# Performance work log

Measured on AMD Instinct MI355X. Metric: run time of the kernel, lower is better.

Reference implementation:

```python
import jax, jax.numpy as jnp
from jax import lax
import numpy as np

K_IN, K_OUT, H, ML = 32, 16, 256, 80
L_PRE, L_FWD, B = 60, 80, 1024


def gru_cell(x, h, Wih, Whh, bih, bhh):
    # torch GRU gate order: r, z, n
    gi = x @ Wih.T + bih
    gh = h @ Whh.T + bhh
    ir, iz, inn = jnp.split(gi, 3, axis=-1)
    hr, hz, hn = jnp.split(gh, 3, axis=-1)
    r = jax.nn.sigmoid(ir + hr)
    z = jax.nn.sigmoid(iz + hz)
    n = jnp.tanh(inn + r * hn)
    return (1.0 - z) * n + z * h


def setup_inputs() -> dict:
    key = jax.random.key(0)
    ks = jax.random.split(key, 24)
    s = 0.05
    rn = lambda k, shp: (jax.random.normal(k, shp) * s).astype(jnp.float32)
    inp = {
        "pre_x": jax.random.normal(ks[0], (L_PRE, B, K_IN), dtype=jnp.float32),
        "pre_y": jax.random.normal(ks[1], (L_PRE, B, K_OUT), dtype=jnp.float32),
        "forward_x": jax.random.normal(ks[2], (L_FWD, B, K_IN), dtype=jnp.float32),
        # encoder: embedding Linear(k_in+k_out -> H), GRU(H,H)
        "enc_emb_W": rn(ks[3], (H, K_IN + K_OUT)),
        "enc_emb_b": rn(ks[4], (H,)),
        "enc_Wih": rn(ks[5], (3 * H, H)),
        "enc_Whh": rn(ks[6], (3 * H, H)),
        "enc_bih": rn(ks[7], (3 * H,)),
        "enc_bhh": rn(ks[8], (3 * H,)),
        # decoder: embedding Linear(k_out+k_in -> H), attn Linear(2H -> ML),
        # attn_combine Linear(2H -> H), GRU(H,H), out Linear(H -> k_out)
        "dec_emb_W": rn(ks[9], (H, K_OUT + K_IN)),
        "dec_emb_b": rn(ks[10], (H,)),
        "attn_W": rn(ks[11], (ML, 2 * H)),
        "attn_b": rn(ks[12], (ML,)),
        "comb_W": rn(ks[13], (H, 2 * H)),
        "comb_b": rn(ks[14], (H,)),
        "dec_Wih": rn(ks[15], (3 * H, H)),
        "dec_Whh": rn(ks[16], (3 * H, H)),
        "dec_bih": rn(ks[17], (3 * H,)),
        "dec_bhh": rn(ks[18], (3 * H,)),
        "out_W": rn(ks[19], (K_OUT, H)),
        "out_b": rn(ks[20], (K_OUT,)),
    }
    return inp


def reference(pre_x, pre_y, forward_x,
              enc_emb_W, enc_emb_b, enc_Wih, enc_Whh, enc_bih, enc_bhh,
              dec_emb_W, dec_emb_b, attn_W, attn_b, comb_W, comb_b,
              dec_Wih, dec_Whh, dec_bih, dec_bhh, out_W, out_b):
    L_pre, batch, _ = pre_x.shape
    hdim = enc_emb_b.shape[0]
    max_len = attn_b.shape[0]

    # ---- encoder ----
    emb = jnp.concatenate([pre_x, pre_y], axis=2) @ enc_emb_W.T + enc_emb_b  # [L_pre,B,H]
    h0 = jnp.zeros((batch, hdim), dtype=pre_x.dtype)

    def enc_step(h, x):
        h2 = gru_cell(x, h, enc_Wih, enc_Whh, enc_bih, enc_bhh)
        return h2, h2

    enc_h, enc_outs = lax.scan(enc_step, h0, emb)
    # pad encoder outputs to max_length along time (zeros beyond L_pre)
    enc_outputs = jnp.zeros((max_len, batch, hdim), dtype=pre_x.dtype).at[:L_pre].set(enc_outs)
    enc_bmh = enc_outputs.transpose(1, 0, 2)  # [B, ML, H]

    # ---- decoder (dropout inactive: eval mode) ----
    def dec_step(carry, fx):
        y, h = carry
        di = jnp.concatenate([y, fx], axis=-1)            # [B, k_out+k_in]
        e = di @ dec_emb_W.T + dec_emb_b                   # [B, H]
        logits = jnp.concatenate([e, h], axis=-1) @ attn_W.T + attn_b  # [B, ML]
        aw = jax.nn.softmax(logits, axis=-1)
        ctx = jnp.einsum('bm,bmh->bh', aw, enc_bmh)        # [B, H]
        g = jnp.tanh(jnp.concatenate([e, ctx], axis=-1) @ comb_W.T + comb_b)
        h2 = gru_cell(g, h, dec_Wih, dec_Whh, dec_bih, dec_bhh)
        y2 = h2 @ out_W.T + out_b                          # [B, k_out]
        return (y2, h2), y2

    y_init = jnp.zeros_like(pre_y[0])
    _, ys = lax.scan(dec_step, (y_init, enc_h), forward_x)
    return ys  # [L_fwd, B, k_out]
```

## Files before the change

### kernel.cpp

```cpp
#include <hip/hip_runtime.h>
#include <hip/hip_bf16.h>

#define BATCH 1024
#define HD 256
#define MLEN 80
#define LPRE 60
#define LFWD 80
#define KIN 32
#define KOUT 16

typedef unsigned short bf16_t;
typedef __attribute__((ext_vector_type(8))) short bf16x8;
typedef __attribute__((ext_vector_type(4))) float f32x4;
typedef __attribute__((ext_vector_type(4))) unsigned u32x4;

#define MFMA __builtin_amdgcn_mfma_f32_16x16x32_bf16

__device__ __forceinline__ float bf2f(bf16_t v){ return __uint_as_float(((unsigned)v)<<16); }
__device__ __forceinline__ bf16_t f2bf(float f){
    unsigned u = __float_as_uint(f);
    return (bf16_t)((u + 0x7FFFu + ((u>>16)&1u)) >> 16);
}
__device__ __forceinline__ unsigned pack2(float lo, float hi){
    return (unsigned)f2bf(lo) | ((unsigned)f2bf(hi)<<16);
}
__device__ __forceinline__ float bflo(unsigned d){ return __uint_as_float(d<<16); }
__device__ __forceinline__ float bfhi(unsigned d){ return __uint_as_float(d & 0xffff0000u); }
__device__ __forceinline__ float sigm(float x){ return 1.0f/(1.0f+__expf(-x)); }

#define OFF_Z  262144
#define OFF_IN 524288
#define OFF_HN 655360

__global__ void pack_gru(const float* __restrict__ Wih, const float* __restrict__ Whh,
                         bf16_t* __restrict__ dst)
{
    int T = blockIdx.x*256 + threadIdx.x;
    int grp, local;
    if (T < 16384){ grp=0; local=T; }
    else if (T < 32768){ grp=1; local=T-16384; }
    else if (T < 40960){ grp=2; local=T-32768; }
    else { grp=3; local=T-40960; }
    int nkt = (grp<2)?16:8;
    int nt  = local / (nkt*64);
    int rem = local - nt*(nkt*64);
    int kt  = rem >> 6;
    int l   = rem & 63;
    int n   = nt*16 + (l&15);
    int k0  = kt*32 + ((l>>4)<<3);
    unsigned w[4];
    #pragma unroll
    for (int h2=0; h2<4; h2++){
        float v[2];
        #pragma unroll
        for (int s=0; s<2; s++){
            int k = k0 + h2*2 + s;
            if (grp==0)      v[s] = (k<256)? Wih[(size_t)n*HD + k]       : Whh[(size_t)n*HD + (k-256)];
            else if (grp==1) v[s] = (k<256)? Wih[(size_t)(256+n)*HD + k] : Whh[(size_t)(256+n)*HD + (k-256)];
            else if (grp==2) v[s] = Wih[(size_t)(512+n)*HD + k];
            else             v[s] = Whh[(size_t)(512+n)*HD + k];
        }
        w[h2] = pack2(v[0], v[1]);
    }
    uint4 u = {w[0],w[1],w[2],w[3]};
    *(uint4*)((char*)dst + (size_t)T*16) = u;
}

__global__ void pack_B512(const float* __restrict__ W, bf16_t* __restrict__ dst)
{
    int T = blockIdx.x*256 + threadIdx.x;
    int nt = T >> 10, kt = (T>>6)&15, l = T&63;
    int n = nt*16 + (l&15);
    int k0 = kt*32 + ((l>>4)<<3);
    unsigned w[4];
    #pragma unroll
    for (int h2=0; h2<4; h2++)
        w[h2] = pack2(W[(size_t)n*512 + k0+h2*2], W[(size_t)n*512 + k0+h2*2+1]);
    uint4 u = {w[0],w[1],w[2],w[3]};
    *(uint4*)((char*)dst + (size_t)T*16) = u;
}

__global__ void wfuse_kernel(const float* __restrict__ dembW, const float* __restrict__ dembB,
                             const float* __restrict__ outW, const float* __restrict__ outB,
                             float* __restrict__ Wfuse, float* __restrict__ ebias)
{
    int T = blockIdx.x*256 + threadIdx.x;
    if (T < 65536){
        int k = T >> 8, n = T & 255;
        float acc = 0.f;
        #pragma unroll
        for (int o=0;o<16;o++) acc += dembW[(size_t)n*48 + o]*outW[(size_t)o*HD + k];
        Wfuse[(size_t)k*HD + n] = acc;
    } else if (T < 65792){
        int n = T - 65536;
        float acc = dembB[n];
        #pragma unroll
        for (int o=0;o<16;o++) acc += outB[o]*dembW[(size_t)n*48 + o];
        ebias[n] = acc;
    }
}

__global__ void pack_logits(const float* __restrict__ Wfuse, const float* __restrict__ dembW,
                            const float* __restrict__ attW, const float* __restrict__ attB,
                            const float* __restrict__ dembB, const float* __restrict__ ebias,
                            bf16_t* __restrict__ BL, bf16_t* __restrict__ BL0,
                            float* __restrict__ lb, float* __restrict__ lb0)
{
    int T = blockIdx.x*256 + threadIdx.x;
    if (T < 5760){
        int variant = (T < 2880) ? 0 : 1;
        int local = variant ? (T-2880) : T;
        int nt = local/576, rem = local - nt*576;
        int kt = rem >> 6, l = rem & 63;
        int m  = nt*16 + (l&15);
        int k0 = kt*32 + ((l>>4)<<3);
        float acc[8];
        if (kt < 8){
            #pragma unroll
            for (int d=0;d<8;d++) acc[d] = attW[(size_t)m*512 + 256 + k0 + d];
            if (variant == 0){
                const float* ar = attW + (size_t)m*512;
                for (int n=0;n<256;n+=4){
                    float4 w = *(const float4*)(ar + n);
                    #pragma unroll
                    for (int d=0;d<8;d++){
                        float4 f = *(const float4*)(Wfuse + (size_t)(k0+d)*HD + n);
                        acc[d] = fmaf(f.x, w.x, acc[d]);
                        acc[d] = fmaf(f.y, w.y, acc[d]);
                        acc[d] = fmaf(f.z, w.z, acc[d]);
                        acc[d] = fmaf(f.w, w.w, acc[d]);
                    }
                }
            }
        } else {
            int kp0 = k0 - 256;
            #pragma unroll
            for (int d=0;d<8;d++) acc[d] = 0.f;
            const float* ar = attW + (size_t)m*512;
            for (int n=0;n<256;n++){
                float w = ar[n];
                const float* dr = dembW + (size_t)n*48 + 16 + kp0;
                float4 d0 = *(const float4*)dr;
                float4 d1 = *(const float4*)(dr+4);
                acc[0]=fmaf(d0.x,w,acc[0]); acc[1]=fmaf(d0.y,w,acc[1]);
                acc[2]=fmaf(d0.z,w,acc[2]); acc[3]=fmaf(d0.w,w,acc[3]);
                acc[4]=fmaf(d1.x,w,acc[4]); acc[5]=fmaf(d1.y,w,acc[5]);
                acc[6]=fmaf(d1.z,w,acc[6]); acc[7]=fmaf(d1.w,w,acc[7]);
            }
        }
        unsigned w4[4];
        #pragma unroll
        for (int h2=0;h2<4;h2++) w4[h2] = pack2(acc[h2*2], acc[h2*2+1]);
        uint4 u = {w4[0],w4[1],w4[2],w4[3]};
        bf16_t* d = variant ? BL0 : BL;
        *(uint4*)((char*)d + (size_t)local*16) = u;
    } else if (T < 5840){
        int m = T - 5760;
        float acc = attB[m];
        const float* ar = attW + (size_t)m*512;
        for (int n=0;n<256;n+=4){
            float4 w = *(const float4*)(ar + n);
            float4 e = *(const float4*)(ebias + n);
            acc = fmaf(e.x,w.x,acc); acc = fmaf(e.y,w.y,acc);
            acc = fmaf(e.z,w.z,acc); acc = fmaf(e.w,w.w,acc);
        }
        lb[m] = acc;
    } else if (T < 5920){
        int m = T - 5840;
        float acc = attB[m];
        const float* ar = attW + (size_t)m*512;
        for (int n=0;n<256;n+=4){
            float4 w = *(const float4*)(ar + n);
            float4 e = *(const float4*)(dembB + n);
            acc = fmaf(e.x,w.x,acc); acc = fmaf(e.y,w.y,acc);
            acc = fmaf(e.z,w.z,acc); acc = fmaf(e.w,w.w,acc);
        }
        lb0[m] = acc;
    }
}

__global__ void pack_gfold(const float* __restrict__ Wfuse, const float* __restrict__ dembW,
                           const float* __restrict__ combW, const float* __restrict__ combB,
                           const float* __restrict__ ebias, const float* __restrict__ dembB,
                           bf16_t* __restrict__ dst, float* __restrict__ cbf, float* __restrict__ cbf0)
{
    int T = blockIdx.x*256 + threadIdx.x;
    if (T < 9216){
        int nt = T/576, rem = T - nt*576;
        int kt = rem >> 6, l = rem & 63;
        int n = nt*16 + (l&15);
        int k0 = kt*32 + ((l>>4)<<3);
        float acc[8];
        #pragma unroll
        for (int d=0;d<8;d++) acc[d] = 0.f;
        const float* wr = combW + (size_t)n*512;
        if (kt < 8){
            for (int j=0;j<256;j+=4){
                float4 w = *(const float4*)(wr + j);
                #pragma unroll
                for (int d=0;d<8;d++){
                    float4 f = *(const float4*)(Wfuse + (size_t)(k0+d)*HD + j);
                    acc[d] = fmaf(f.x, w.x, acc[d]);
                    acc[d] = fmaf(f.y, w.y, acc[d]);
                    acc[d] = fmaf(f.z, w.z, acc[d]);
                    acc[d] = fmaf(f.w, w.w, acc[d]);
                }
            }
        } else {
            int kp0 = k0 - 256;
            for (int j=0;j<256;j++){
                float w = wr[j];
                const float* dr = dembW + (size_t)j*48 + 16 + kp0;
                float4 d0 = *(const float4*)dr;
                float4 d1 = *(const float4*)(dr+4);
                acc[0]=fmaf(d0.x,w,acc[0]); acc[1]=fmaf(d0.y,w,acc[1]);
                acc[2]=fmaf(d0.z,w,acc[2]); acc[3]=fmaf(d0.w,w,acc[3]);
                acc[4]=fmaf(d1.x,w,acc[4]); acc[5]=fmaf(d1.y,w,acc[5]);
                acc[6]=fmaf(d1.z,w,acc[6]); acc[7]=fmaf(d1.w,w,acc[7]);
            }
        }
        unsigned w4[4];
        #pragma unroll
        for (int h2=0;h2<4;h2++) w4[h2] = pack2(acc[h2*2], acc[h2*2+1]);
        uint4 u = {w4[0],w4[1],w4[2],w4[3]};
        *(uint4*)((char*)dst + (size_t)T*16) = u;
    } else if (T < 9472){
        int n = T - 9216;
        float acc = combB[n];
        const float* wr = combW + (size_t)n*512;
        for (int j=0;j<256;j+=4){
            float4 w = *(const float4*)(wr + j);
            float4 e = *(const float4*)(ebias + j);
            acc = fmaf(e.x,w.x,acc); acc = fmaf(e.y,w.y,acc);
            acc = fmaf(e.z,w.z,acc); acc = fmaf(e.w,w.w,acc);
        }
        cbf[n] = acc;
    } else if (T < 9728){
        int n = T - 9472;
        float acc = combB[n];
        const float* wr = combW + (size_t)n*512;
        for (int j=0;j<256;j+=4){
            float4 w = *(const float4*)(wr + j);
            float4 e = *(const float4*)(dembB + j);
            acc = fmaf(e.x,w.x,acc); acc = fmaf(e.y,w.y,acc);
            acc = fmaf(e.z,w.z,acc); acc = fmaf(e.w,w.w,acc);
        }
        cbf0[n] = acc;
    }
}

__global__ void pack_out(const float* __restrict__ outW, bf16_t* __restrict__ dst)
{
    int T = blockIdx.x*256 + threadIdx.x;
    int kt = T >> 6, l = T & 63;
    int n  = l & 15;
    int k0 = kt*32 + ((l>>4)<<3);
    unsigned w[4];
    #pragma unroll
    for (int h2=0; h2<4; h2++)
        w[h2] = pack2(outW[(size_t)n*HD + k0+h2*2], outW[(size_t)n*HD + k0+h2*2+1]);
    uint4 u = {w[0],w[1],w[2],w[3]};
    *(uint4*)((char*)dst + (size_t)T*16) = u;
}

__global__ __launch_bounds__(256) void emb_kernel(
    const float* __restrict__ px, const float* __restrict__ py,
    const float* __restrict__ embW, const float* __restrict__ embB,
    bf16_t* __restrict__ emb)
{
    __shared__ float Ws[256*49];
    __shared__ float xy[16][48];
    __shared__ float bs[256];
    int t = blockIdx.y, b0 = blockIdx.x*16, tid = threadIdx.x;
    for (int i = tid; i < 256*48; i += 256){ int n=i/48, k=i-n*48; Ws[n*49+k]=embW[i]; }
    bs[tid] = embB[tid];
    for (int i = tid; i < 16*48; i += 256){
        int r=i/48, k=i-r*48;
        xy[r][k] = (k<KIN)? px[((size_t)t*BATCH + b0+r)*KIN + k]
                          : py[((size_t)t*BATCH + b0+r)*KOUT + (k-KIN)];
    }
    __syncthreads();
    int n = tid;
    const float* w = &Ws[n*49];
    for (int r=0;r<16;r++){
        float acc = bs[n];
        #pragma unroll
        for (int k=0;k<48;k++) acc += xy[r][k]*w[k];
        emb[((size_t)t*BATCH + b0+r)*HD + n] = f2bf(acc);
    }
}

__global__ void fxconv(const float* __restrict__ fx, bf16_t* __restrict__ dst)
{
    size_t i = (size_t)blockIdx.x*256 + threadIdx.x;
    const float4* s = (const float4*)(fx + i*8);
    float4 a = s[0], b = s[1];
    uint4 u = { pack2(a.x,a.y), pack2(a.z,a.w), pack2(b.x,b.y), pack2(b.z,b.w) };
    *(uint4*)(dst + i*8) = u;
}

__global__ __launch_bounds__(256) void pgemm(
    const bf16_t* __restrict__ enc, const bf16_t* __restrict__ Bcmb,
    bf16_t* __restrict__ P)
{
    __shared__ __align__(16) bf16_t As[16][264];
    __shared__ __align__(16) bf16_t Gs[16][264];
    int tid = threadIdx.x, b0 = blockIdx.x*16, t = blockIdx.y;
    const bf16_t* src = enc + ((size_t)t*BATCH + b0)*HD;
    for (int i = tid; i < 512; i += 256){
        int r = i>>5, c = i&31;
        *(uint4*)&As[r][c*8] = *(const uint4*)(src + (size_t)r*HD + c*8);
    }
    __syncthreads();
    int lane = tid&63, wave = tid>>6;
    const bf16_t* arow = &As[lane&15][(lane>>4)*8];
    size_t loff = (size_t)lane*16;
    #pragma unroll
    for (int u=0; u<4; u++){
        int nt = wave*4 + u;
        f32x4 c = {0,0,0,0};
        #pragma unroll
        for (int k8=0; k8<8; k8++){
            bf16x8 a = *(const bf16x8*)(arow + k8*32);
            bf16x8 b = *(const bf16x8*)((const char*)Bcmb + (size_t)(((nt<<4)+8+k8)<<10) + loff);
            c = MFMA(a, b, c, 0,0,0);
        }
        int n = (nt<<4) + (lane&15);
        #pragma unroll
        for (int q=0;q<4;q++) Gs[((lane>>4)<<2)+q][n] = f2bf(c[q]);
    }
    __syncthreads();
    bf16_t* dst = P + ((size_t)t*BATCH + b0)*HD;
    for (int i = tid; i < 512; i += 256){
        int r = i>>5, c = i&31;
        *(uint4*)(dst + (size_t)r*HD + c*8) = *(const uint4*)&Gs[r][c*8];
    }
}

__global__ __launch_bounds__(512) void gru_step2(
    const bf16_t* __restrict__ A0, const bf16_t* __restrict__ A1,
    const bf16_t* __restrict__ Bp,
    const float* __restrict__ bih, const float* __restrict__ bhh,
    const float* __restrict__ hprev, float* __restrict__ hnext,
    bf16_t* __restrict__ hnext_bf, bf16_t* __restrict__ extra_bf)
{
    __shared__ __align__(16) bf16_t As[16][520];
    __shared__ __align__(16) f32x4 redR[4][64];
    __shared__ __align__(16) f32x4 redZ[4][64];
    __shared__ __align__(16) f32x4 redI[4][64];
    int tid = threadIdx.x, b0 = blockIdx.x*16;
    for (int i = tid; i < 1024; i += 512){
        int r = i>>6, c = i&63;
        const bf16_t* src = (c<32)? (A0 + (size_t)(b0+r)*HD + c*8)
                                  : (A1 + (size_t)(b0+r)*HD + (c-32)*8);
        *(uint4*)&As[r][c*8] = *(const uint4*)src;
    }
    __syncthreads();
    int lane = tid & 63, wave = tid >> 6;
    int pairId = wave >> 1, half = wave & 1;
    int jt = blockIdx.y*4 + pairId;
    const char* arow = (const char*)&As[lane&15][(lane>>4)*8];
    const char* bpc = (const char*)Bp;
    size_t loff = (size_t)lane*16;
    size_t offX = half ? (size_t)OFF_HN : (size_t)OFF_IN;
    int kt0 = half*8;
    f32x4 cr={0,0,0,0}, cz={0,0,0,0}, cx={0,0,0,0};
    #pragma unroll
    for (int k8=0; k8<8; k8++){
        int kt = kt0 + k8;
        bf16x8 a  = *(const bf16x8*)(arow + kt*64);
        bf16x8 br = *(const bf16x8*)(bpc + (size_t)(((jt<<4)+kt)<<10) + loff);
        bf16x8 bz = *(const bf16x8*)(bpc + OFF_Z + (size_t)(((jt<<4)+kt)<<10) + loff);
        bf16x8 bx = *(const bf16x8*)(bpc + offX + (size_t)(((jt<<3)+k8)<<10) + loff);
        cr = MFMA(a, br, cr, 0,0,0);
        cz = MFMA(a, bz, cz, 0,0,0);
        cx = MFMA(a, bx, cx, 0,0,0);
    }
    if (half == 0){
        redR[pairId][lane] = cr;
        redZ[pairId][lane] = cz;
        redI[pairId][lane] = cx;
    }
    __syncthreads();
    if (half == 1){
        f32x4 crA = redR[pairId][lane];
        f32x4 czA = redZ[pairId][lane];
        f32x4 ci  = redI[pairId][lane];
        int j = (jt<<4) + (lane&15);
        float b_r = bih[j] + bhh[j];
        float b_z = bih[256+j] + bhh[256+j];
        float b_i = bih[512+j], b_h = bhh[512+j];
        #pragma unroll
        for (int q=0;q<4;q++){
            int b = b0 + ((lane>>4)<<2) + q;
            float rv = sigm(cr[q] + crA[q] + b_r);
            float zv = sigm(cz[q] + czA[q] + b_z);
            float nv = tanhf(ci[q] + b_i + rv*(cx[q] + b_h));
            float h2 = (1.0f - zv)*nv + zv*hprev[(size_t)b*HD + j];
            hnext[(size_t)b*HD + j] = h2;
            bf16_t hb = f2bf(h2);
            hnext_bf[(size_t)b*HD + j] = hb;
            extra_bf[(size_t)b*HD + j] = hb;
        }
    }
}

__global__ __launch_bounds__(1024) void dec_front(
    const bf16_t* __restrict__ hbf, const bf16_t* __restrict__ fxt,
    const bf16_t* __restrict__ P,
    const bf16_t* __restrict__ BL, const bf16_t* __restrict__ Bgf,
    const bf16_t* __restrict__ Bout,
    const float* __restrict__ lbp, const float* __restrict__ cbf,
    const float* __restrict__ outB,
    int t, bf16_t* __restrict__ g_out, float* __restrict__ out)
{
    __shared__ __align__(16) bf16_t As[16][296];
    __shared__ float awL[16][84];
    __shared__ float Cpart[16][256];
    __shared__ float CbF[16][260];

    int tid = threadIdx.x, b0 = blockIdx.x*16;

    if (tid < 576){
        int r = tid/36, c = tid - r*36;
        const bf16_t* src = (c<32)? (hbf + (size_t)(b0+r)*HD + c*8)
                                  : (fxt + (size_t)(b0+r)*KIN + (c-32)*8);
        *(uint4*)&As[r][c*8] = *(const uint4*)src;
    }

    int half = tid >> 9;
    int u    = tid & 511;
    int cr_  = u >> 5;
    int cc0  = (u & 31) * 8;
    const bf16_t* cbp = P + ((size_t)(half*30)*BATCH + (b0+cr_))*HD + cc0;
    u32x4 pf[10];
    #pragma unroll
    for (int i=0;i<10;i++) pf[i] = *(const u32x4*)(cbp + (size_t)i*BATCH*HD);

    __syncthreads();

    int lane = tid & 63, wave = tid >> 6;
    const bf16_t* arow = &As[lane&15][(lane>>4)*8];
    size_t loff = (size_t)lane*16;
    int kt0 = t ? 0 : 8;

    if (wave < 5){
        f32x4 c = {0,0,0,0};
        #pragma unroll
        for (int kt = 0; kt < 9; kt++){
            bf16x8 a = *(const bf16x8*)(arow + kt*32);
            bf16x8 b = *(const bf16x8*)((const char*)BL + (size_t)((wave*9+kt)<<10) + loff);
            c = MFMA(a, b, c, 0,0,0);
        }
        int m = (wave<<4) + (lane&15);
        float bbm = lbp[m];
        #pragma unroll
        for (int q=0;q<4;q++) awL[((lane>>4)<<2)+q][m] = c[q] + bbm;
    } else if (wave == 5 && t > 0){
        f32x4 c = {0,0,0,0};
        #pragma unroll
        for (int kt = 0; kt < 8; kt++){
            bf16x8 a = *(const bf16x8*)(arow + kt*32);
            bf16x8 b = *(const bf16x8*)((const char*)Bout + (size_t)(kt<<10) + loff);
            c = MFMA(a, b, c, 0,0,0);
        }
        int o = lane & 15;
        float bo = outB[o];
        #pragma unroll
        for (int q=0;q<4;q++){
            int r = ((lane>>4)<<2) + q;
            out[((size_t)(t-1)*BATCH + b0+r)*KOUT + o] = c[q] + bo;
        }
    }
    __syncthreads();

    if (tid < 256){
        int r2 = tid >> 4, l2 = tid & 15;
        float vmax = -1e30f;
        for (int m=l2; m<80; m+=16) vmax = fmaxf(vmax, awL[r2][m]);
        #pragma unroll
        for (int k=1; k<16; k<<=1) vmax = fmaxf(vmax, __shfl_xor(vmax, k, 16));
        float ps = 0.f;
        for (int m=l2; m<80; m+=16){ float v = __expf(awL[r2][m]-vmax); awL[r2][m]=v; ps += v; }
        #pragma unroll
        for (int k=1; k<16; k<<=1) ps += __shfl_xor(ps, k, 16);
        float inv = 1.0f/ps;
        for (int m=l2; m<80; m+=16) awL[r2][m] *= inv;
    }
    __syncthreads();

    float acc[8];
    #pragma unroll
    for (int i=0;i<8;i++) acc[i] = 0.f;
    {
        const float* awr = &awL[cr_][half*30];
        #pragma unroll
        for (int i=0;i<10;i++){
            float w = awr[i];
            acc[0]=fmaf(w,bflo(pf[i][0]),acc[0]); acc[1]=fmaf(w,bfhi(pf[i][0]),acc[1]);
            acc[2]=fmaf(w,bflo(pf[i][1]),acc[2]); acc[3]=fmaf(w,bfhi(pf[i][1]),acc[3]);
            acc[4]=fmaf(w,bflo(pf[i][2]),acc[4]); acc[5]=fmaf(w,bfhi(pf[i][2]),acc[5]);
            acc[6]=fmaf(w,bflo(pf[i][3]),acc[6]); acc[7]=fmaf(w,bfhi(pf[i][3]),acc[7]);
        }
        #pragma unroll 5
        for (int i=10;i<30;i++){
            u32x4 v = *(const u32x4*)(cbp + (size_t)i*BATCH*HD);
            float w = awr[i];
            acc[0]=fmaf(w,bflo(v[0]),acc[0]); acc[1]=fmaf(w,bfhi(v[0]),acc[1]);
            acc[2]=fmaf(w,bflo(v[1]),acc[2]); acc[3]=fmaf(w,bfhi(v[1]),acc[3]);
            acc[4]=fmaf(w,bflo(v[2]),acc[4]); acc[5]=fmaf(w,bfhi(v[2]),acc[5]);
            acc[6]=fmaf(w,bflo(v[3]),acc[6]); acc[7]=fmaf(w,bfhi(v[3]),acc[7]);
        }
    }
    if (half == 0){
        float4 p0 = {acc[0],acc[1],acc[2],acc[3]};
        float4 p1 = {acc[4],acc[5],acc[6],acc[7]};
        *(float4*)&Cpart[cr_][cc0]   = p0;
        *(float4*)&Cpart[cr_][cc0+4] = p1;
    }
    __syncthreads();

    if (half == 1){
        float4 p0 = *(const float4*)&Cpart[cr_][cc0];
        float4 p1 = *(const float4*)&Cpart[cr_][cc0+4];
        float4 o0 = {acc[0]+p0.x, acc[1]+p0.y, acc[2]+p0.z, acc[3]+p0.w};
        float4 o1 = {acc[4]+p1.x, acc[5]+p1.y, acc[6]+p1.z, acc[7]+p1.w};
        *(float4*)&CbF[cr_][cc0]   = o0;
        *(float4*)&CbF[cr_][cc0+4] = o1;
    }
    __syncthreads();

    {
        f32x4 c = {0,0,0,0};
        for (int kt=kt0; kt<9; kt++){
            bf16x8 a = *(const bf16x8*)(arow + kt*32);
            bf16x8 b = *(const bf16x8*)((const char*)Bgf + (size_t)((wave*9+kt)<<10) + loff);
            c = MFMA(a, b, c, 0,0,0);
        }
        int n = (wave<<4) + (lane&15);
        float bb = cbf[n];
        #pragma unroll
        for (int q=0;q<4;q++){
            int r = ((lane>>4)<<2) + q;
            g_out[(size_t)(b0+r)*HD + n] = f2bf(tanhf(c[q] + CbF[r][n] + bb));
        }
    }
}

__global__ __launch_bounds__(256) void final79(
    const float* __restrict__ hf, const float* __restrict__ outW,
    const float* __restrict__ outB, float* __restrict__ ys)
{
    __shared__ float hs[16][260];
    __shared__ float ow[16*260];
    int tid = threadIdx.x, b0 = blockIdx.x*16;
    for (int i=tid;i<4096;i+=256){ int o2=i>>8,k=i&255; ow[o2*260+k]=outW[(size_t)o2*HD+k]; }
    for (int i=tid;i<4096;i+=256){ int r=i>>8,k=i&255; hs[r][k]=hf[(size_t)(b0+r)*HD+k]; }
    __syncthreads();
    int r=tid>>4, o=tid&15;
    float acc=outB[o];
    const float* w=&ow[o*260];
    for(int k=0;k<256;k++) acc += hs[r][k]*w[k];
    ys[((size_t)79*BATCH + b0+r)*KOUT + o] = acc;
}

extern "C" void kernel_launch(void* const* d_in, const int* in_sizes, int n_in,
                              void* d_out, int out_size, void* d_ws, size_t ws_size,
                              hipStream_t stream) {
    const float* pre_x    = (const float*)d_in[0];
    const float* pre_y    = (const float*)d_in[1];
    const float* fwd_x    = (const float*)d_in[2];
    const float* enc_embW = (const float*)d_in[3];
    const float* enc_embB = (const float*)d_in[4];
    const float* enc_Wih  = (const float*)d_in[5];
    const float* enc_Whh  = (const float*)d_in[6];
    const float* enc_bih  = (const float*)d_in[7];
    const float* enc_bhh  = (const float*)d_in[8];
    const float* dec_embW = (const float*)d_in[9];
    const float* dec_embB = (const float*)d_in[10];
    const float* attn_W   = (const float*)d_in[11];
    const float* attn_b   = (const float*)d_in[12];
    const float* comb_W   = (const float*)d_in[13];
    const float* comb_b   = (const float*)d_in[14];
    const float* dec_Wih  = (const float*)d_in[15];
    const float* dec_Whh  = (const float*)d_in[16];
    const float* dec_bih  = (const float*)d_in[17];
    const float* dec_bhh  = (const float*)d_in[18];
    const float* out_W    = (const float*)d_in[19];
    const float* out_b    = (const float*)d_in[20];
    float* out = (float*)d_out;

    char* ws = (char*)d_ws;
    size_t o = 0;
    auto alloc = [&](size_t bytes)->char*{
        char* p = ws + o; o = (o + bytes + 255) & ~(size_t)255; return p;
    };
    bf16_t* EMB     = (bf16_t*)alloc((size_t)LPRE*BATCH*HD*2);
    bf16_t* ENC_OUT = (bf16_t*)alloc((size_t)LPRE*BATCH*HD*2);
    bf16_t* PBUF    = (bf16_t*)alloc((size_t)LPRE*BATCH*HD*2);
    bf16_t* FXB     = (bf16_t*)alloc((size_t)LFWD*BATCH*KIN*2);
    float*  HF0     = (float*) alloc((size_t)BATCH*HD*4);
    float*  HF1     = (float*) alloc((size_t)BATCH*HD*4);
    bf16_t* HB0     = (bf16_t*)alloc((size_t)BATCH*HD*2);
    bf16_t* HB1     = (bf16_t*)alloc((size_t)BATCH*HD*2);
    bf16_t* GBUF    = (bf16_t*)alloc((size_t)BATCH*HD*2);
    bf16_t* DUMMY   = (bf16_t*)alloc((size_t)BATCH*HD*2);
    float*  WFUSE   = (float*) alloc((size_t)256*256*4);
    float*  EBIAS   = (float*) alloc(256*4);
    float*  LB      = (float*) alloc(80*4);
    float*  LB0     = (float*) alloc(80*4);
    float*  CBF     = (float*) alloc(256*4);
    float*  CBF0    = (float*) alloc(256*4);
    bf16_t* PACK_ENC = (bf16_t*)alloc(786432);
    bf16_t* PACK_DEC = (bf16_t*)alloc(786432);
    bf16_t* PACK_CMB = (bf16_t*)alloc(262144);
    bf16_t* PACK_GF  = (bf16_t*)alloc(147456);
    bf16_t* PACK_BL  = (bf16_t*)alloc(46080);
    bf16_t* PACK_BL0 = (bf16_t*)alloc(46080);
    bf16_t* PACK_OUT = (bf16_t*)alloc(8192);

    hipMemsetAsync(HF0, 0, (size_t)BATCH*HD*4, stream);
    hipMemsetAsync(HB0, 0, (size_t)BATCH*HD*2, stream);

    dim3 blk(256);
    emb_kernel<<<dim3(64,60), blk, 0, stream>>>(pre_x, pre_y, enc_embW, enc_embB, EMB);
    fxconv<<<dim3(1280), blk, 0, stream>>>(fwd_x, FXB);
    pack_gru<<<dim3(192), blk, 0, stream>>>(enc_Wih, enc_Whh, PACK_ENC);
    pack_gru<<<dim3(192), blk, 0, stream>>>(dec_Wih, dec_Whh, PACK_DEC);
    pack_B512<<<dim3(64), blk, 0, stream>>>(comb_W, PACK_CMB);
    wfuse_kernel<<<dim3(257), blk, 0, stream>>>(dec_embW, dec_embB, out_W, out_b, WFUSE, EBIAS);
    pack_logits<<<dim3(24), blk, 0, stream>>>(WFUSE, dec_embW, attn_W, attn_b, dec_embB,
                                              EBIAS, PACK_BL, PACK_BL0, LB, LB0);
    pack_gfold<<<dim3(38), blk, 0, stream>>>(WFUSE, dec_embW, comb_W, comb_b,
                                             EBIAS, dec_embB, PACK_GF, CBF, CBF0);
    pack_out<<<dim3(2), blk, 0, stream>>>(out_W, PACK_OUT);

    float*  HF[2] = {HF0, HF1};
    bf16_t* HB[2] = {HB0, HB1};
    int p = 0;

    for (int t = 0; t < LPRE; t++){
        gru_step2<<<dim3(64,4), dim3(512), 0, stream>>>(
            EMB + (size_t)t*BATCH*HD, HB[p], PACK_ENC, enc_bih, enc_bhh,
            HF[p], HF[p^1], HB[p^1], ENC_OUT + (size_t)t*BATCH*HD);
        p ^= 1;
    }
    pgemm<<<dim3(64,60), blk, 0, stream>>>(ENC_OUT, PACK_CMB, PBUF);

    for (int t = 0; t < LFWD; t++){
        const bf16_t* fxt = FXB + (size_t)t*BATCH*KIN;
        dec_front<<<dim3(64), dim3(1024), 0, stream>>>(
            HB[p], fxt, PBUF,
            t ? PACK_BL : PACK_BL0, PACK_GF, PACK_OUT,
            t ? LB : LB0, t ? CBF : CBF0, out_b,
            t, GBUF, out);
        gru_step2<<<dim3(64,4), dim3(512), 0, stream>>>(
            GBUF, HB[p], PACK_DEC, dec_bih, dec_bhh,
            HF[p], HF[p^1], HB[p^1], DUMMY);
        p ^= 1;
    }
    final79<<<dim3(64), blk, 0, stream>>>(HF[p], out_W, out_b, out);
}
```

Baseline: 2.275 ms.

## Fuse encoder GRU time loop into one persistent kernel with state in LDS

Replaces the per-timestep encoder GRU launches with a single persistent kernel in which each block owns 16 batch rows for all 60 steps. The hidden state stays in shared memory (fp32 and bf16 copies), and the next step's embedding row is loaded into LDS. This removes 60 kernel launches and the global round-trips of the hidden state. The cost is less parallelism: only 64 blocks, each re-streaming the full packed GRU weights from L2 every step.

```diff
diff --git a/kernel.cpp b/kernel.cpp
--- a/kernel.cpp
+++ b/kernel.cpp
@@ -299,6 +299,87 @@
     *(uint4*)(dst + i*8) = u;
 }
 
+__global__ __launch_bounds__(1024) void enc_persist(
+    const bf16_t* __restrict__ EMB, const bf16_t* __restrict__ Bp,
+    const float* __restrict__ bih, const float* __restrict__ bhh,
+    float* __restrict__ hf_out, bf16_t* __restrict__ hb_out,
+    bf16_t* __restrict__ enc_out)
+{
+    __shared__ __align__(16) bf16_t Xb[16][264];
+    __shared__ __align__(16) bf16_t Hb[16][264];
+    __shared__ float Hf[16][260];
+    int tid = threadIdx.x, b0 = blockIdx.x*16;
+    int lane = tid & 63, wave = tid >> 6;
+    size_t loff = (size_t)lane*16;
+    const char* bpc = (const char*)Bp;
+
+    for (int i = tid; i < 16*264; i += 1024) ((bf16_t*)Hb)[i] = 0;
+    for (int i = tid; i < 16*260; i += 1024) ((float*)Hf)[i] = 0.f;
+    if (tid < 512){
+        int r = tid >> 5, c0 = (tid & 31)*8;
+        *(uint4*)&Xb[r][c0] = *(const uint4*)&EMB[((size_t)0*BATCH + b0+r)*HD + c0];
+    }
+    __syncthreads();
+
+    int jt = wave;
+    int j = (jt<<4) + (lane&15);
+    float b_r = bih[j] + bhh[j];
+    float b_z = bih[256+j] + bhh[256+j];
+    float b_i = bih[512+j], b_h = bhh[512+j];
+    const bf16_t* ar = &Xb[lane&15][(lane>>4)*8];
+    const bf16_t* ah = &Hb[lane&15][(lane>>4)*8];
+
+    #pragma unroll 1
+    for (int t = 0; t < LPRE; t++){
+        f32x4 cr={0,0,0,0}, cz={0,0,0,0}, ci={0,0,0,0}, ch={0,0,0,0};
+        #pragma unroll
+        for (int kt=0; kt<16; kt++){
+            bf16x8 a = (kt<8)? *(const bf16x8*)(ar + kt*32)
+                             : *(const bf16x8*)(ah + (kt-8)*32);
+            bf16x8 br = *(const bf16x8*)(bpc + (size_t)(((jt<<4)+kt)<<10) + loff);
+            bf16x8 bz = *(const bf16x8*)(bpc + OFF_Z + (size_t)(((jt<<4)+kt)<<10) + loff);
+            cr = MFMA(a, br, cr, 0,0,0);
+            cz = MFMA(a, bz, cz, 0,0,0);
+            if (kt < 8){
+                bf16x8 bi = *(const bf16x8*)(bpc + OFF_IN + (size_t)(((jt<<3)+kt)<<10) + loff);
+                ci = MFMA(a, bi, ci, 0,0,0);
+            } else {
+                bf16x8 bh2 = *(const bf16x8*)(bpc + OFF_HN + (size_t)(((jt<<3)+kt-8)<<10) + loff);
+                ch = MFMA(a, bh2, ch, 0,0,0);
+            }
+        }
+        __syncthreads();
+        #pragma unroll
+        for (int q=0;q<4;q++){
+            int r = ((lane>>4)<<2) + q;
+            float rv = sigm(cr[q] + b_r);
+            float zv = sigm(cz[q] + b_z);
+            float nv = tanhf(ci[q] + b_i + rv*(ch[q] + b_h));
+            float h2 = (1.0f - zv)*nv + zv*Hf[r][j];
+            Hf[r][j] = h2;
+            Hb[r][j] = f2bf(h2);
+        }
+        __syncthreads();
+        if (tid < 512){
+            int r = tid >> 5, c0 = (tid & 31)*8;
+            *(uint4*)(enc_out + ((size_t)t*BATCH + b0+r)*HD + c0) = *(const uint4*)&Hb[r][c0];
+            if (t+1 < LPRE)
+                *(uint4*)&Xb[r][c0] = *(const uint4*)&EMB[((size_t)(t+1)*BATCH + b0+r)*HD + c0];
+        }
+        __syncthreads();
+    }
+
+    if (tid < 512){
+        int r = tid >> 5, c0 = (tid & 31)*8;
+        *(uint4*)&hb_out[(size_t)(b0+r)*HD + c0] = *(const uint4*)&Hb[r][c0];
+    }
+    {
+        int r = tid >> 6, c0 = (tid & 63)*4;
+        float4 v = {Hf[r][c0], Hf[r][c0+1], Hf[r][c0+2], Hf[r][c0+3]};
+        *(float4*)&hf_out[(size_t)(b0+r)*HD + c0] = v;
+    }
+}
+
 __global__ __launch_bounds__(256) void pgemm(
     const bf16_t* __restrict__ enc, const bf16_t* __restrict__ Bcmb,
     bf16_t* __restrict__ P)
@@ -619,9 +700,6 @@
     bf16_t* PACK_BL0 = (bf16_t*)alloc(46080);
     bf16_t* PACK_OUT = (bf16_t*)alloc(8192);
 
-    hipMemsetAsync(HF0, 0, (size_t)BATCH*HD*4, stream);
-    hipMemsetAsync(HB0, 0, (size_t)BATCH*HD*2, stream);
-
     dim3 blk(256);
     emb_kernel<<<dim3(64,60), blk, 0, stream>>>(pre_x, pre_y, enc_embW, enc_embB, EMB);
     fxconv<<<dim3(1280), blk, 0, stream>>>(fwd_x, FXB);
@@ -635,17 +713,14 @@
                                              EBIAS, dec_embB, PACK_GF, CBF, CBF0);
     pack_out<<<dim3(2), blk, 0, stream>>>(out_W, PACK_OUT);
 
+    enc_persist<<<dim3(64), dim3(1024), 0, stream>>>(
+        EMB, PACK_ENC, enc_bih, enc_bhh, HF0, HB0, ENC_OUT);
+
+    pgemm<<<dim3(64,60), blk, 0, stream>>>(ENC_OUT, PACK_CMB, PBUF);
+
     float*  HF[2] = {HF0, HF1};
     bf16_t* HB[2] = {HB0, HB1};
     int p = 0;
-
-    for (int t = 0; t < LPRE; t++){
-        gru_step2<<<dim3(64,4), dim3(512), 0, stream>>>(
-            EMB + (size_t)t*BATCH*HD, HB[p], PACK_ENC, enc_bih, enc_bhh,
-            HF[p], HF[p^1], HB[p^1], ENC_OUT + (size_t)t*BATCH*HD);
-        p ^= 1;
-    }
-    pgemm<<<dim3(64,60), blk, 0, stream>>>(ENC_OUT, PACK_CMB, PBUF);
 
     for (int t = 0; t < LFWD; t++){
         const bf16_t* fxt = FXB + (size_t)t*BATCH*KIN;
```

New measurement: 2.770 ms. 1.22x slower.

## Split decoder front kernel across two column-half blocks per batch tile

Applied to the files above, without the earlier changes.

The decoder front kernel now launches a 64x2 grid, with each block handling half of the 256 hidden columns for the context accumulation and the combine GEMM. The attention logits and softmax are recomputed redundantly in both blocks, and only the y==0 block writes the output projection. This doubles the number of blocks in flight (64 blocks underfill the GPU) and halves per-thread context loads, at the cost of duplicated attention work and half the waves sitting idle in the final MFMA stage.

```diff
diff --git a/kernel.cpp b/kernel.cpp
--- a/kernel.cpp
+++ b/kernel.cpp
@@ -405,7 +405,7 @@
     }
 }
 
-__global__ __launch_bounds__(1024) void dec_front(
+__global__ __launch_bounds__(1024) void dec_front2(
     const bf16_t* __restrict__ hbf, const bf16_t* __restrict__ fxt,
     const bf16_t* __restrict__ P,
     const bf16_t* __restrict__ BL, const bf16_t* __restrict__ Bgf,
@@ -416,10 +416,10 @@
 {
     __shared__ __align__(16) bf16_t As[16][296];
     __shared__ float awL[16][84];
-    __shared__ float Cpart[16][256];
-    __shared__ float CbF[16][260];
-
-    int tid = threadIdx.x, b0 = blockIdx.x*16;
+    __shared__ float Cpart[16][128];
+    __shared__ float CbF[16][132];
+
+    int tid = threadIdx.x, b0 = blockIdx.x*16, y = blockIdx.y;
 
     if (tid < 576){
         int r = tid/36, c = tid - r*36;
@@ -431,11 +431,11 @@
     int half = tid >> 9;
     int u    = tid & 511;
     int cr_  = u >> 5;
-    int cc0  = (u & 31) * 8;
-    const bf16_t* cbp = P + ((size_t)(half*30)*BATCH + (b0+cr_))*HD + cc0;
-    u32x4 pf[10];
+    int cl4  = (u & 31) * 4;
+    const bf16_t* cbp = P + ((size_t)(half*30)*BATCH + (b0+cr_))*HD + y*128 + cl4;
+    uint2 pf[10];
     #pragma unroll
-    for (int i=0;i<10;i++) pf[i] = *(const u32x4*)(cbp + (size_t)i*BATCH*HD);
+    for (int i=0;i<10;i++) pf[i] = *(const uint2*)(cbp + (size_t)i*BATCH*HD);
 
     __syncthreads();
 
@@ -456,7 +456,7 @@
         float bbm = lbp[m];
         #pragma unroll
         for (int q=0;q<4;q++) awL[((lane>>4)<<2)+q][m] = c[q] + bbm;
-    } else if (wave == 5 && t > 0){
+    } else if (wave == 5 && y == 0 && t > 0){
         f32x4 c = {0,0,0,0};
         #pragma unroll
         for (int kt = 0; kt < 8; kt++){
@@ -489,60 +489,51 @@
     }
     __syncthreads();
 
-    float acc[8];
-    #pragma unroll
-    for (int i=0;i<8;i++) acc[i] = 0.f;
+    float a0=0.f, a1=0.f, a2=0.f, a3=0.f;
     {
         const float* awr = &awL[cr_][half*30];
         #pragma unroll
         for (int i=0;i<10;i++){
             float w = awr[i];
-            acc[0]=fmaf(w,bflo(pf[i][0]),acc[0]); acc[1]=fmaf(w,bfhi(pf[i][0]),acc[1]);
-            acc[2]=fmaf(w,bflo(pf[i][1]),acc[2]); acc[3]=fmaf(w,bfhi(pf[i][1]),acc[3]);
-            acc[4]=fmaf(w,bflo(pf[i][2]),acc[4]); acc[5]=fmaf(w,bfhi(pf[i][2]),acc[5]);
-            acc[6]=fmaf(w,bflo(pf[i][3]),acc[6]); acc[7]=fmaf(w,bfhi(pf[i][3]),acc[7]);
+            a0=fmaf(w,bflo(pf[i].x),a0); a1=fmaf(w,bfhi(pf[i].x),a1);
+            a2=fmaf(w,bflo(pf[i].y),a2); a3=fmaf(w,bfhi(pf[i].y),a3);
         }
         #pragma unroll 5
         for (int i=10;i<30;i++){
-            u32x4 v = *(const u32x4*)(cbp + (size_t)i*BATCH*HD);
+            uint2 v = *(const uint2*)(cbp + (size_t)i*BATCH*HD);
             float w = awr[i];
-            acc[0]=fmaf(w,bflo(v[0]),acc[0]); acc[1]=fmaf(w,bfhi(v[0]),acc[1]);
-            acc[2]=fmaf(w,bflo(v[1]),acc[2]); acc[3]=fmaf(w,bfhi(v[1]),acc[3]);
-            acc[4]=fmaf(w,bflo(v[2]),acc[4]); acc[5]=fmaf(w,bfhi(v[2]),acc[5]);
-            acc[6]=fmaf(w,bflo(v[3]),acc[6]); acc[7]=fmaf(w,bfhi(v[3]),acc[7]);
+            a0=fmaf(w,bflo(v.x),a0); a1=fmaf(w,bfhi(v.x),a1);
+            a2=fmaf(w,bflo(v.y),a2); a3=fmaf(w,bfhi(v.y),a3);
         }
     }
     if (half == 0){
-        float4 p0 = {acc[0],acc[1],acc[2],acc[3]};
-        float4 p1 = {acc[4],acc[5],acc[6],acc[7]};
-        *(float4*)&Cpart[cr_][cc0]   = p0;
-        *(float4*)&Cpart[cr_][cc0+4] = p1;
+        float4 p = {a0,a1,a2,a3};
+        *(float4*)&Cpart[cr_][cl4] = p;
     }
     __syncthreads();
 
     if (half == 1){
-        float4 p0 = *(const float4*)&Cpart[cr_][cc0];
-        float4 p1 = *(const float4*)&Cpart[cr_][cc0+4];
-        float4 o0 = {acc[0]+p0.x, acc[1]+p0.y, acc[2]+p0.z, acc[3]+p0.w};
-        float4 o1 = {acc[4]+p1.x, acc[5]+p1.y, acc[6]+p1.z, acc[7]+p1.w};
-        *(float4*)&CbF[cr_][cc0]   = o0;
-        *(float4*)&CbF[cr_][cc0+4] = o1;
-    }
-    __syncthreads();
-
-    {
+        float4 p = *(const float4*)&Cpart[cr_][cl4];
+        float4 o0 = {a0+p.x, a1+p.y, a2+p.z, a3+p.w};
+        *(float4*)&CbF[cr_][cl4] = o0;
+    }
+    __syncthreads();
+
+    if (wave < 8){
+        int nt = y*8 + wave;
         f32x4 c = {0,0,0,0};
         for (int kt=kt0; kt<9; kt++){
             bf16x8 a = *(const bf16x8*)(arow + kt*32);
-            bf16x8 b = *(const bf16x8*)((const char*)Bgf + (size_t)((wave*9+kt)<<10) + loff);
+            bf16x8 b = *(const bf16x8*)((const char*)Bgf + (size_t)((nt*9+kt)<<10) + loff);
             c = MFMA(a, b, c, 0,0,0);
         }
-        int n = (wave<<4) + (lane&15);
+        int n  = (nt<<4) + (lane&15);
+        int nl = (wave<<4) + (lane&15);
         float bb = cbf[n];
         #pragma unroll
         for (int q=0;q<4;q++){
             int r = ((lane>>4)<<2) + q;
-            g_out[(size_t)(b0+r)*HD + n] = f2bf(tanhf(c[q] + CbF[r][n] + bb));
+            g_out[(size_t)(b0+r)*HD + n] = f2bf(tanhf(c[q] + CbF[r][nl] + bb));
         }
     }
 }
@@ -649,7 +640,7 @@
 
     for (int t = 0; t < LFWD; t++){
         const bf16_t* fxt = FXB + (size_t)t*BATCH*KIN;
-        dec_front<<<dim3(64), dim3(1024), 0, stream>>>(
+        dec_front2<<<dim3(64,2), dim3(1024), 0, stream>>>(
             HB[p], fxt, PBUF,
             t ? PACK_BL : PACK_BL0, PACK_GF, PACK_OUT,
             t ? LB : LB0, t ? CBF : CBF0, out_b,
```

Result: faster. 2.123 ms (-6.7%).
